# Performance work log

Hardware: AMD Instinct MI355X
Metric: run time of the kernel (lower is better)

The kernel has to match this reference:

```python
import jax, jax.numpy as jnp
from jax import lax
import numpy as np

DN = ('NCHW', 'OIHW', 'NCHW')
K = 5          # downsample_kernel_size
S = 2          # scale_factor
M = 64         # m_channels


def setup_inputs() -> dict:
    key = jax.random.key(0)
    k0, k1, k2 = jax.random.split(key, 3)
    B, C, H, W = 8, 256, 128, 128
    x = jax.random.normal(k0, (B, C, H, W), jnp.float32)
    # compress_conv: 1x1, C -> M
    w1 = jax.random.normal(k1, (M, C, 1, 1), jnp.float32) * (1.0 / np.sqrt(C))
    b1 = jnp.zeros((M,), jnp.float32)
    # encoder_conv: 3x3, M -> K*K, stride S, pad 1
    w2 = jax.random.normal(k2, (K * K, M, 3, 3), jnp.float32) * (1.0 / np.sqrt(M * 9))
    b2 = jnp.zeros((K * K,), jnp.float32)
    return {"x": x, "w1": w1, "b1": b1, "w2": w2, "b2": b2}


def reference(x, w1, b1, w2, b2):
    B, C, H, W = x.shape
    nH, nW = H // S, W // S
    # kernel prediction branch
    ker = lax.conv_general_dilated(x, w1, (1, 1), 'VALID', dimension_numbers=DN)
    ker = ker + b1[None, :, None, None]
    ker = lax.conv_general_dilated(ker, w2, (S, S), ((1, 1), (1, 1)), dimension_numbers=DN)
    ker = ker + b2[None, :, None, None]          # (B, K*K, nH, nW)
    ker = jax.nn.softmax(ker, axis=1)
    # unfold: (B, C*K*K, nH, nW), channel-major patch ordering (matches torch Unfold)
    pad = K // 2
    patches = lax.conv_general_dilated_patches(
        x, (K, K), (S, S), ((pad, pad), (pad, pad)), dimension_numbers=DN)
    patches = patches.reshape(B, C, K * K, nH, nW)
    # softmax-weighted sum over the K*K window per output pixel
    return jnp.einsum('bckhw,bkhw->bchw', patches, ker)
```

## Files before the change

kernel.cpp:

```cpp
#include <hip/hip_runtime.h>
#include <hip/hip_bf16.h>

#define Bq 8
#define Cq 256
#define Hq 128
#define Wq 128
#define Mq 64
#define KK 25
#define NH 64
#define NW 64
#define HWq (Hq*Wq)
#define NHW (NH*NW)

typedef __attribute__((ext_vector_type(8))) short short8;
typedef __attribute__((ext_vector_type(4))) float f32x4;

__device__ __forceinline__ unsigned short f2b(float f) {
  __hip_bfloat16 h = __float2bfloat16(f);
  return __builtin_bit_cast(unsigned short, h);
}

#define XPAD 72
__global__ __launch_bounds__(256) void conv1x1_mfma(
    const float* __restrict__ x, const float* __restrict__ w1,
    const float* __restrict__ b1, float* __restrict__ t1) {
  __shared__ unsigned short xs[128 * XPAD];
  __shared__ unsigned short ws[64 * XPAD];
  const int tid  = threadIdx.x;
  const int lane = tid & 63;
  const int wv   = tid >> 6;
  const int P0   = blockIdx.x << 7;
  const int b    = P0 >> 14;
  const int hw0  = P0 & (HWq - 1);

  const int quad = lane >> 4;
  const int l15  = lane & 15;

  const int sc  = tid >> 2;
  const int sp0 = (tid & 3) * 4;
  const int wm  = tid >> 2;
  const int wc0 = (tid & 3) * 16;

  f32x4 acc[4][2];
#pragma unroll
  for (int mt = 0; mt < 4; ++mt)
#pragma unroll
    for (int nt = 0; nt < 2; ++nt) acc[mt][nt] = (f32x4)0.f;

  for (int cc = 0; cc < 4; ++cc) {
    __syncthreads();
    const float* xgc = x + ((size_t)b * Cq + cc * 64 + sc) * HWq + hw0 + sp0;
#pragma unroll
    for (int i = 0; i < 8; ++i) {
      float4 v = *(const float4*)(xgc + i * 16);
      int px = sp0 + i * 16;
      xs[(px + 0) * XPAD + sc] = f2b(v.x);
      xs[(px + 1) * XPAD + sc] = f2b(v.y);
      xs[(px + 2) * XPAD + sc] = f2b(v.z);
      xs[(px + 3) * XPAD + sc] = f2b(v.w);
    }
    const float* wgc = w1 + wm * Cq + cc * 64 + wc0;
#pragma unroll
    for (int u = 0; u < 4; ++u) {
      float4 v = *(const float4*)(wgc + u * 4);
      unsigned short* d = &ws[wm * XPAD + wc0 + u * 4];
      d[0] = f2b(v.x); d[1] = f2b(v.y); d[2] = f2b(v.z); d[3] = f2b(v.w);
    }
    __syncthreads();
#pragma unroll
    for (int ks = 0; ks < 2; ++ks) {
      const int c0 = ks * 32 + quad * 8;
      short8 af[4], bfr[2];
#pragma unroll
      for (int mt = 0; mt < 4; ++mt)
        af[mt] = *(const short8*)&ws[(mt * 16 + l15) * XPAD + c0];
#pragma unroll
      for (int nt = 0; nt < 2; ++nt)
        bfr[nt] = *(const short8*)&xs[(wv * 32 + nt * 16 + l15) * XPAD + c0];
#pragma unroll
      for (int mt = 0; mt < 4; ++mt)
#pragma unroll
        for (int nt = 0; nt < 2; ++nt)
          acc[mt][nt] = __builtin_amdgcn_mfma_f32_16x16x32_bf16(
              af[mt], bfr[nt], acc[mt][nt], 0, 0, 0);
    }
  }
#pragma unroll
  for (int mt = 0; mt < 4; ++mt) {
#pragma unroll
    for (int r = 0; r < 4; ++r) {
      int m = mt * 16 + quad * 4 + r;
      float bv = b1[m];
#pragma unroll
      for (int nt = 0; nt < 2; ++nt) {
        int px = wv * 32 + nt * 16 + l15;
        t1[((size_t)b * Mq + m) * HWq + hw0 + px] = acc[mt][nt][r] + bv;
      }
    }
  }
}

__global__ __launch_bounds__(512) void encoder_kernel(
    const float* __restrict__ t1, const float* __restrict__ w2,
    const float* __restrict__ b2, float* __restrict__ ker) {
  __shared__ float red[8][KK][64];
  const int tid = threadIdx.x;
  const int ow  = tid & 63;
  const int mg  = tid >> 6;
  const int b   = blockIdx.x >> 6;
  const int oh  = blockIdx.x & 63;

  float acc[KK];
#pragma unroll
  for (int k = 0; k < KK; ++k) acc[k] = 0.f;

  const float* tb = t1 + (size_t)b * Mq * HWq;
  const int iwb = 2 * ow - 1;

  for (int mi = 0; mi < 8; ++mi) {
    const int m = __builtin_amdgcn_readfirstlane(mg * 8 + mi);
    const float* tm = tb + (size_t)m * HWq;
    const float* wm = w2 + m * 9;
#pragma unroll
    for (int dh = 0; dh < 3; ++dh) {
      int ih = 2 * oh + dh - 1;
      if ((unsigned)ih < (unsigned)Hq) {
        const float* tr = tm + ih * Wq;
        float v0 = (ow > 0) ? tr[iwb] : 0.f;
        float v1 = tr[iwb + 1];
        float v2 = tr[iwb + 2];
        const float* wr = wm + dh * 3;
#pragma unroll
        for (int k = 0; k < KK; ++k) {
          acc[k] += v0 * wr[k * 576 + 0];
          acc[k] += v1 * wr[k * 576 + 1];
          acc[k] += v2 * wr[k * 576 + 2];
        }
      }
    }
  }
#pragma unroll
  for (int k = 0; k < KK; ++k) red[mg][k][ow] = acc[k];
  __syncthreads();
  if (tid < 64) {
    float lg[KK];
#pragma unroll
    for (int k = 0; k < KK; ++k) {
      float s = b2[k];
#pragma unroll
      for (int g = 0; g < 8; ++g) s += red[g][k][tid];
      lg[k] = s;
    }
    float mx = lg[0];
#pragma unroll
    for (int k = 1; k < KK; ++k) mx = fmaxf(mx, lg[k]);
    float s = 0.f;
#pragma unroll
    for (int k = 0; k < KK; ++k) { lg[k] = __expf(lg[k] - mx); s += lg[k]; }
    float inv = 1.f / s;
    float* kb = ker + (size_t)b * KK * NHW + oh * NW + tid;
#pragma unroll
    for (int k = 0; k < KK; ++k) kb[k * NHW] = lg[k] * inv;
  }
}

#define RSL_ROWS 19
#define RSL_CSZ  (RSL_ROWS * Wq)
__global__ __launch_bounds__(256) void reassemble_kernel(
    const float* __restrict__ x, const float* __restrict__ ker,
    float* __restrict__ out) {
  __shared__ float xsl[8 * RSL_CSZ + 8];
  const int tid = threadIdx.x;
  const int bid = blockIdx.x;
  const int cg  = bid & 31;
  const int ohg = (bid >> 5) & 7;
  const int b   = bid >> 8;
  const int r0  = 16 * ohg - 2;

  const int zlo = (r0 < 0) ? -r0 : 0;
  const int zhi = (r0 + RSL_ROWS > Hq) ? (r0 + RSL_ROWS - Hq) : 0;
  if (zlo > 0) {
    for (int c = 0; c < 8; ++c)
      for (int i = tid; i < zlo * Wq; i += 256) xsl[c * RSL_CSZ + i] = 0.f;
  }
  if (zhi > 0) {
    for (int c = 0; c < 8; ++c)
      for (int i = tid; i < zhi * Wq; i += 256)
        xsl[c * RSL_CSZ + (RSL_ROWS - zhi) * Wq + i] = 0.f;
  }
  const int vs = (r0 > 0) ? r0 : 0;
  const int ve = (r0 + RSL_ROWS < Hq) ? (r0 + RSL_ROWS) : Hq;
  const int nvec = ((ve - vs) * Wq) >> 2;
  const int loff = (vs - r0) * Wq;
  for (int c = 0; c < 8; ++c) {
    const float* g = x + ((size_t)(b * Cq + cg * 8 + c)) * HWq + vs * Wq;
    float* d = xsl + c * RSL_CSZ + loff;
    for (int i = tid; i < nvec; i += 256) {
      float4 v = *(const float4*)(g + 4 * i);
      *(float4*)(d + 4 * i) = v;
    }
  }

  const int ow = tid & 63;
  const int rq = tid >> 6;
  const int oh = 8 * ohg + 2 * rq;
  float kr0[KK], kr1[KK];
  const float* kb = ker + (size_t)b * KK * NHW + oh * NW + ow;
#pragma unroll
  for (int k = 0; k < KK; ++k) { kr0[k] = kb[k * NHW]; kr1[k] = kb[k * NHW + NW]; }

  __syncthreads();

  const int jb = 4 * rq;
  const bool e0 = (ow > 0);
  const bool e4 = (ow < 63);
  const float2 z2 = make_float2(0.f, 0.f);

  for (int c = 0; c < 8; ++c) {
    const float* sl = xsl + c * RSL_CSZ;
    float a0 = 0.f, a1 = 0.f;
#pragma unroll
    for (int j = 0; j < 7; ++j) {
      const float* xr = sl + (jb + j) * Wq + 2 * ow - 2;
      float2 v01 = e0 ? *(const float2*)xr : z2;
      float2 v23 = *(const float2*)(xr + 2);
      float  v4  = e4 ? xr[4] : 0.f;
      if (j < 5) {
        a0 += v01.x * kr0[j*5+0]; a0 += v01.y * kr0[j*5+1];
        a0 += v23.x * kr0[j*5+2]; a0 += v23.y * kr0[j*5+3];
        a0 += v4    * kr0[j*5+4];
      }
      if (j >= 2) {
        int dy = j - 2;
        a1 += v01.x * kr1[dy*5+0]; a1 += v01.y * kr1[dy*5+1];
        a1 += v23.x * kr1[dy*5+2]; a1 += v23.y * kr1[dy*5+3];
        a1 += v4    * kr1[dy*5+4];
      }
    }
    float* op = out + ((size_t)(b * Cq + cg * 8 + c)) * NHW + oh * NW + ow;
    op[0]  = a0;
    op[NW] = a1;
  }
}

extern "C" void kernel_launch(void* const* d_in, const int* in_sizes, int n_in,
                              void* d_out, int out_size, void* d_ws, size_t ws_size,
                              hipStream_t stream) {
  const float* x  = (const float*)d_in[0];
  const float* w1 = (const float*)d_in[1];
  const float* b1 = (const float*)d_in[2];
  const float* w2 = (const float*)d_in[3];
  const float* b2 = (const float*)d_in[4];
  float* out = (float*)d_out;

  float* t1  = (float*)d_ws;
  float* ker = t1 + (size_t)Bq * Mq * HWq;

  conv1x1_mfma<<<1024, 256, 0, stream>>>(x, w1, b1, t1);
  encoder_kernel<<<Bq * NH, 512, 0, stream>>>(t1, w2, b2, ker);
  reassemble_kernel<<<2048, 256, 0, stream>>>(x, ker, out);
}
```

Measured before the change: 301.4 us.

## Prefetch x into registers, double-buffer per-wave LDS, preload full w1 once

The conv1x1 kernel now stages all of w1 (64x256 bf16) into LDS once, instead of reloading a slice every channel chunk. Each wave writes its own 32-pixel x tile into a double-buffered LDS slot, so the block-wide __syncthreads in the loop go away. Loads for the next channel chunk are issued into registers before the MFMAs of the current chunk, and bf16 values are packed two per 32-bit store. This trades more LDS and register use, which may lower occupancy, for fewer barriers and better load/compute overlap.

```diff
diff --git a/kernel.cpp b/kernel.cpp
--- a/kernel.cpp
+++ b/kernel.cpp
@@ -19,13 +19,17 @@
   __hip_bfloat16 h = __float2bfloat16(f);
   return __builtin_bit_cast(unsigned short, h);
 }
-
-#define XPAD 72
+__device__ __forceinline__ unsigned int pk2(float a, float b) {
+  return (unsigned int)f2b(a) | ((unsigned int)f2b(b) << 16);
+}
+
+#define WS_STR 280
+#define XS_STR 80
 __global__ __launch_bounds__(256) void conv1x1_mfma(
     const float* __restrict__ x, const float* __restrict__ w1,
     const float* __restrict__ b1, float* __restrict__ t1) {
-  __shared__ unsigned short xs[128 * XPAD];
-  __shared__ unsigned short ws[64 * XPAD];
+  __shared__ unsigned short wsl[64 * WS_STR];
+  __shared__ unsigned short xsl[2][4][32 * XS_STR];
   const int tid  = threadIdx.x;
   const int lane = tid & 63;
   const int wv   = tid >> 6;
@@ -36,10 +40,24 @@
   const int quad = lane >> 4;
   const int l15  = lane & 15;
 
-  const int sc  = tid >> 2;
-  const int sp0 = (tid & 3) * 4;
-  const int wm  = tid >> 2;
-  const int wc0 = (tid & 3) * 16;
+  {
+    const int m  = tid >> 2;
+    const int cb = (tid & 3) * 64;
+    const float* wg = w1 + m * Cq + cb;
+    unsigned int* wu = (unsigned int*)&wsl[m * WS_STR + cb];
+#pragma unroll
+    for (int u = 0; u < 16; ++u) {
+      float4 v = *(const float4*)(wg + 4 * u);
+      wu[2 * u]     = pk2(v.x, v.y);
+      wu[2 * u + 1] = pk2(v.z, v.w);
+    }
+  }
+  __syncthreads();
+
+  const int cp = lane >> 1;
+  const int pg = lane & 1;
+  const float* xb = x + (size_t)b * Cq * HWq + hw0 + wv * 32 + pg * 16;
+  unsigned int* xu = (unsigned int*)&xsl[0][0][0];
 
   f32x4 acc[4][2];
 #pragma unroll
@@ -47,36 +65,45 @@
 #pragma unroll
     for (int nt = 0; nt < 2; ++nt) acc[mt][nt] = (f32x4)0.f;
 
+  float4 cur[8];
+  {
+    const float* g = xb + (size_t)(2 * cp) * HWq;
+#pragma unroll
+    for (int u = 0; u < 4; ++u) cur[u]     = *(const float4*)(g + 4 * u);
+#pragma unroll
+    for (int u = 0; u < 4; ++u) cur[4 + u] = *(const float4*)(g + HWq + 4 * u);
+  }
+
   for (int cc = 0; cc < 4; ++cc) {
-    __syncthreads();
-    const float* xgc = x + ((size_t)b * Cq + cc * 64 + sc) * HWq + hw0 + sp0;
-#pragma unroll
-    for (int i = 0; i < 8; ++i) {
-      float4 v = *(const float4*)(xgc + i * 16);
-      int px = sp0 + i * 16;
-      xs[(px + 0) * XPAD + sc] = f2b(v.x);
-      xs[(px + 1) * XPAD + sc] = f2b(v.y);
-      xs[(px + 2) * XPAD + sc] = f2b(v.z);
-      xs[(px + 3) * XPAD + sc] = f2b(v.w);
-    }
-    const float* wgc = w1 + wm * Cq + cc * 64 + wc0;
-#pragma unroll
-    for (int u = 0; u < 4; ++u) {
-      float4 v = *(const float4*)(wgc + u * 4);
-      unsigned short* d = &ws[wm * XPAD + wc0 + u * 4];
-      d[0] = f2b(v.x); d[1] = f2b(v.y); d[2] = f2b(v.z); d[3] = f2b(v.w);
-    }
-    __syncthreads();
+    {
+      unsigned int* d = xu + ((cc & 1) * 4 + wv) * 1280 + cp;
+#pragma unroll
+      for (int u = 0; u < 4; ++u) {
+        int px0 = pg * 16 + 4 * u;
+        d[(px0 + 0) * 40] = pk2(cur[u].x, cur[4 + u].x);
+        d[(px0 + 1) * 40] = pk2(cur[u].y, cur[4 + u].y);
+        d[(px0 + 2) * 40] = pk2(cur[u].z, cur[4 + u].z);
+        d[(px0 + 3) * 40] = pk2(cur[u].w, cur[4 + u].w);
+      }
+    }
+    if (cc < 3) {
+      const float* g = xb + (size_t)((cc + 1) * 64 + 2 * cp) * HWq;
+#pragma unroll
+      for (int u = 0; u < 4; ++u) cur[u]     = *(const float4*)(g + 4 * u);
+#pragma unroll
+      for (int u = 0; u < 4; ++u) cur[4 + u] = *(const float4*)(g + HWq + 4 * u);
+    }
+    const unsigned short* xw = &xsl[cc & 1][wv][0];
 #pragma unroll
     for (int ks = 0; ks < 2; ++ks) {
       const int c0 = ks * 32 + quad * 8;
       short8 af[4], bfr[2];
 #pragma unroll
       for (int mt = 0; mt < 4; ++mt)
-        af[mt] = *(const short8*)&ws[(mt * 16 + l15) * XPAD + c0];
+        af[mt] = *(const short8*)&wsl[(mt * 16 + l15) * WS_STR + cc * 64 + c0];
 #pragma unroll
       for (int nt = 0; nt < 2; ++nt)
-        bfr[nt] = *(const short8*)&xs[(wv * 32 + nt * 16 + l15) * XPAD + c0];
+        bfr[nt] = *(const short8*)&xw[(nt * 16 + l15) * XS_STR + c0];
 #pragma unroll
       for (int mt = 0; mt < 4; ++mt)
 #pragma unroll
@@ -85,6 +112,7 @@
               af[mt], bfr[nt], acc[mt][nt], 0, 0, 0);
     }
   }
+
 #pragma unroll
   for (int mt = 0; mt < 4; ++mt) {
 #pragma unroll
```

New measurement: 298.3 us. About the same (-1.0%).
